# Kernel tuning notes

Measured on AMD Instinct MI355X. Metric: run time of the kernel, lower is better.

Reference implementation:

```python
import jax, jax.numpy as jnp
import numpy as np

SEED_THR = 0.5
DUP_THR = 0.8


def _connected_labels(adj):
    """Min-label propagation with pointer jumping; adj: [N,N] bool (diag set for active nodes)."""
    N = adj.shape[0]

    def cond(carry):
        _, changed = carry
        return changed

    def body(carry):
        labels, _ = carry
        nbr_min = jnp.min(jnp.where(adj, labels[None, :], N), axis=1)
        new = jnp.minimum(labels, nbr_min)
        new = jnp.minimum(new, new[new])  # pointer jumping -> O(log N) convergence
        return new, jnp.any(new != labels)

    labels0 = jnp.arange(N)
    labels, _ = jax.lax.while_loop(cond, body, (labels0, jnp.array(True)))
    return labels


def _per_image(sig, scores):
    # sig: [N,C], scores: [N]
    N = sig.shape[0]
    idx = jnp.arange(N)
    sel = scores >= SEED_THR
    # fallback: if nothing passes the threshold, select argmax score
    sel = jnp.where(sel.any(), sel, idx == jnp.argmax(scores))

    # cosine pairwise similarity
    sn = sig * jax.lax.rsqrt(jnp.sum(sig * sig, axis=-1, keepdims=True) + 1e-12)
    sim = sn @ sn.T  # [N,N]

    adj = (sim >= DUP_THR) & sel[:, None] & sel[None, :]
    adj = adj | jnp.diag(sel)  # diagonal True for selected nodes

    labels = _connected_labels(adj)  # component root = min node index in component

    neg_inf = jnp.float32(-1e30)
    masked_scores = jnp.where(sel, scores, neg_inf)
    comp_max = jnp.full((N,), neg_inf, dtype=scores.dtype).at[labels].max(masked_scores)
    is_best = sel & (scores >= comp_max[labels])
    # tie-break: smallest index (matches torch argmax-first semantics)
    comp_best = jnp.full((N,), N, dtype=jnp.int32).at[labels].min(
        jnp.where(is_best, idx, N).astype(jnp.int32))
    is_seed = sel & (idx == comp_best[labels])

    # compact seeds to the front, ordered by component root (== DFS discovery order)
    sort_key = jnp.where(is_seed, labels, N)
    order = jnp.argsort(sort_key)
    mask = is_seed[order]  # [N] bool, True for valid seed slots
    seed_sig = jnp.where(mask[:, None], sig[order], jnp.zeros((), sig.dtype))
    seed_sc = jnp.where(mask, scores[order], jnp.zeros((), scores.dtype))
    return seed_sig, mask, seed_sc


def reference(query_signatures, query_seed_logits):
    L, B, Q, C = query_signatures.shape
    sig = jnp.transpose(query_signatures, (1, 0, 2, 3)).reshape(B, L * Q, C)
    logits = jnp.transpose(query_seed_logits, (1, 0, 2)).reshape(B, L * Q).astype(jnp.float32)
    scores = jax.nn.sigmoid(logits)
    seed_signatures, pad_mask, seed_scores = jax.vmap(_per_image)(sig, scores)
    return seed_signatures, pad_mask, seed_scores


def setup_inputs() -> dict:
    key = jax.random.key(0)
    k1, k2 = jax.random.split(key)
    L, B, Q, C = 6, 4, 900, 256
    return {
        "query_signatures": jax.random.normal(k1, (L, B, Q, C), dtype=jnp.float32),
        "query_seed_logits": jax.random.normal(k2, (L, B, Q), dtype=jnp.float32),
    }
```

## Files before the change

kernel.cpp:

```cpp
#include <hip/hip_runtime.h>
#include <cstdint>
#include <cstddef>

#define LDIM 6
#define BDIM 4
#define QDIM 900
#define CDIM 256
#define NDIM (LDIM*QDIM)
#define NN   5408
#define T128 43
#define NT128 (T128*(T128+1)/2)

typedef float floatx4 __attribute__((ext_vector_type(4)));

__device__ __forceinline__ int sig_off(int b, int n) {
    int l = n / QDIM, q = n - l * QDIM;
    return ((l * BDIM + b) * QDIM + q) * CDIM;
}
__device__ __forceinline__ int logit_off(int b, int n) {
    int l = n / QDIM, q = n - l * QDIM;
    return (l * BDIM + b) * QDIM + q;
}

__device__ __forceinline__ int uf_load(const int* p, int i) {
    return __hip_atomic_load(&p[i], __ATOMIC_RELAXED, __HIP_MEMORY_SCOPE_AGENT);
}
__device__ int uf_find(int* p, int x) {
    int r = x;
    int pr = uf_load(p, r);
    while (pr != r) { r = pr; pr = uf_load(p, r); }
    return r;
}
__device__ void uf_union(int* p, int a, int b) {
    int ra = uf_find(p, a), rb = uf_find(p, b);
    while (ra != rb) {
        int hi = ra > rb ? ra : rb;
        int lo = ra ^ rb ^ hi;
        int old = atomicCAS(&p[hi], hi, lo);
        if (old == hi) return;
        ra = uf_find(p, old);
        rb = uf_find(p, lo);
    }
}

__device__ __forceinline__ int pk_fp8x4(float a, float b, float c, float d) {
    int p = __builtin_amdgcn_cvt_pk_fp8_f32(a, b, 0, false);
    p = __builtin_amdgcn_cvt_pk_fp8_f32(c, d, p, true);
    return p;
}

__global__ void k_init(const float* __restrict__ logits, float* __restrict__ scores,
                       int* __restrict__ parent, unsigned long long* __restrict__ compKey,
                       int* __restrict__ selIdx, int* __restrict__ Mcnt,
                       unsigned long long* __restrict__ argKey, int* __restrict__ done) {
    int b = blockIdx.y;
    int n = blockIdx.x * 256 + threadIdx.x;
    int lane = threadIdx.x & 63;
    if (n < NN) compKey[b * NN + n] = 0ULL;
    unsigned long long key = 0ULL;
    int f = 0;
    if (n < NDIM) {
        float x = logits[logit_off(b, n)];
        float sc = 1.0f / (1.0f + expf(-x));
        scores[b * NN + n] = sc;
        parent[b * NN + n] = n;
        f = (sc >= 0.5f) ? 1 : 0;
        key = ((unsigned long long)__float_as_uint(sc) << 32) | (unsigned int)(~n);
    }
    unsigned long long bal = __ballot(f != 0);
    int cnt = __popcll(bal);
    int rank = __popcll(bal & ((1ull << lane) - 1ull));
    int base = 0;
    if (lane == 0 && cnt) base = atomicAdd(&Mcnt[b], cnt);
    base = __shfl(base, 0);
    if (f) selIdx[b * NN + base + rank] = n;
    for (int off = 32; off; off >>= 1) {
        unsigned long long o = __shfl_down(key, off);
        if (o > key) key = o;
    }
    if (lane == 0) atomicMax(&argKey[b], key);
    __syncthreads();
    if (threadIdx.x == 0) {
        int prev = __hip_atomic_fetch_add(&done[b], 1, __ATOMIC_ACQ_REL,
                                          __HIP_MEMORY_SCOPE_AGENT);
        if (prev == (int)gridDim.x - 1) {
            if (__hip_atomic_load(&Mcnt[b], __ATOMIC_RELAXED, __HIP_MEMORY_SCOPE_AGENT) == 0) {
                unsigned long long k = __hip_atomic_load(&argKey[b], __ATOMIC_RELAXED,
                                                         __HIP_MEMORY_SCOPE_AGENT);
                selIdx[b * NN + 0] = (int)(~(unsigned int)(k & 0xffffffffULL));
                __hip_atomic_store(&Mcnt[b], 1, __ATOMIC_RELAXED, __HIP_MEMORY_SCOPE_AGENT);
            }
        }
    }
}

__global__ void k_tobf(const float* __restrict__ sig, const int* __restrict__ selIdx,
                       const int* __restrict__ Mcnt, char* __restrict__ Xf8) {
    int b = blockIdx.y;
    int g = (blockIdx.x * blockDim.x + threadIdx.x) >> 6;
    int lane = threadIdx.x & 63;
    if (g >= Mcnt[b]) return;
    int node = selIdx[b * NN + g];
    const float4 v = *(const float4*)(sig + sig_off(b, node) + lane * 4);
    float s = v.x * v.x + v.y * v.y + v.z * v.z + v.w * v.w;
    for (int off = 32; off; off >>= 1) s += __shfl_down(s, off);
    s = __shfl(s, 0);
    float ninv = rsqrtf(s + 1e-12f);
    int p = pk_fp8x4(v.x * ninv, v.y * ninv, v.z * ninv, v.w * ninv);
    int slot = (lane >> 2) ^ (g & 15);
    *(int*)(Xf8 + ((size_t)(b * NN + g)) * 256 + slot * 16 + (lane & 3) * 4) = p;
}

__global__ __launch_bounds__(256) void k_sim_mfma(const char* __restrict__ Xf8,
                                                  const int* __restrict__ selIdx,
                                                  const int* __restrict__ Mcnt,
                                                  int* __restrict__ parent) {
    int bx = blockIdx.x;
    int b = bx & 3;
    int t = bx >> 2;
    int M = Mcnt[b];
    int ti = (int)((sqrtf(8.0f * (float)t + 1.0f) - 1.0f) * 0.5f);
    while ((ti + 1) * (ti + 2) / 2 <= t) ti++;
    while (ti * (ti + 1) / 2 > t) ti--;
    int tj = t - ti * (ti + 1) / 2;
    if (ti * 128 >= M) return;

    extern __shared__ char Bs[];

    int tid = threadIdx.x;
    int lane = tid & 63, wave = tid >> 6;
    int rsel = lane & 15, quad = lane >> 4;

    const char* xb = Xf8 + ((size_t)b * NN) * 256;
#pragma unroll
    for (int k = 0; k < 8; k++) {
        int i = wave * 8 + k;
        int row = min(tj * 128 + 4 * i, NN - 4);
        const char* src = xb + (size_t)row * 256 + lane * 16;
        __builtin_amdgcn_global_load_lds(
            (const __attribute__((address_space(1))) unsigned int*)src,
            (__attribute__((address_space(3))) unsigned int*)(Bs + i * 1024),
            16, 0, 0);
    }

    int rA = ti * 128 + wave * 32;
    int gA0 = min(rA + rsel, M - 1);
    int gA1 = min(rA + 16 + rsel, M - 1);
    const char* pA0 = Xf8 + ((size_t)(b * NN + gA0)) * 256;
    const char* pA1 = Xf8 + ((size_t)(b * NN + gA1)) * 256;
    int swA0 = gA0 & 15, swA1 = gA1 & 15;

    __syncthreads();

    floatx4 acc[2][8];
#pragma unroll
    for (int s = 0; s < 2; s++)
#pragma unroll
        for (int nj = 0; nj < 8; nj++) acc[s][nj] = (floatx4){0.f, 0.f, 0.f, 0.f};

#pragma unroll
    for (int ks = 0; ks < 8; ks++) {
        int ch = ks * 2 + (quad >> 1);
        int ih = (quad & 1) * 8;
        long a0 = *(const long*)(pA0 + ((ch ^ swA0) << 4) + ih);
        long a1 = *(const long*)(pA1 + ((ch ^ swA1) << 4) + ih);
#pragma unroll
        for (int nj = 0; nj < 8; nj++) {
            int lr = nj * 16 + rsel;
            long bb = *(const long*)(Bs + lr * 256 + (((ch ^ (lr & 15)) << 4) + ih));
            acc[0][nj] = __builtin_amdgcn_mfma_f32_16x16x32_fp8_fp8(a0, bb, acc[0][nj], 0, 0, 0);
            acc[1][nj] = __builtin_amdgcn_mfma_f32_16x16x32_fp8_fp8(a1, bb, acc[1][nj], 0, 0, 0);
        }
    }

#pragma unroll
    for (int s = 0; s < 2; s++) {
        int rowA = rA + s * 16 + quad * 4;
#pragma unroll
        for (int nj = 0; nj < 8; nj++) {
            int gj = tj * 128 + nj * 16 + rsel;
#pragma unroll
            for (int r = 0; r < 4; r++) {
                int gi = rowA + r;
                if (gi < M && gj < M && gi > gj && acc[s][nj][r] >= 0.8f) {
                    uf_union(parent + b * NN, selIdx[b * NN + gi], selIdx[b * NN + gj]);
                }
            }
        }
    }
}

__global__ __launch_bounds__(1024) void k_comp(int* __restrict__ parent,
                                               const int* __restrict__ selIdx,
                                               const int* __restrict__ Mcnt,
                                               const float* __restrict__ scores,
                                               unsigned long long* __restrict__ compKey,
                                               int* __restrict__ seedNode,
                                               int* __restrict__ Scnt) {
    int b = blockIdx.x, t = threadIdx.x;
    int lane = t & 63, w = t >> 6;
    __shared__ int wsum[16];
    __shared__ int sbase;
    if (t == 0) sbase = 0;
    __syncthreads();

    int M = Mcnt[b];
    for (int base = 0; base < M; base += 1024) {
        int g = base + t;
        if (g < M) {
            int node = selIdx[b * NN + g];
            int root = uf_find(parent + b * NN, node);
            unsigned long long key =
                ((unsigned long long)__float_as_uint(scores[b * NN + node]) << 32) |
                (unsigned int)(~node);
            atomicMax(&compKey[b * NN + root], key);
        }
    }
    __syncthreads();

    for (int base = 0; base < NDIM; base += 1024) {
        int n = base + t;
        unsigned long long key = 0ULL;
        if (n < NDIM)
            key = __hip_atomic_load(&compKey[b * NN + n], __ATOMIC_RELAXED,
                                    __HIP_MEMORY_SCOPE_AGENT);
        int f = (key != 0ULL) ? 1 : 0;
        unsigned long long bal = __ballot(f != 0);
        int rank = __popcll(bal & ((1ull << lane) - 1ull));
        if (lane == 0) wsum[w] = __popcll(bal);
        __syncthreads();
        if (t == 0) {
            int s = sbase;
            for (int i = 0; i < 16; i++) { int v = wsum[i]; wsum[i] = s; s += v; }
            sbase = s;
        }
        __syncthreads();
        if (f) seedNode[b * NN + wsum[w] + rank] = (int)(~(unsigned int)(key & 0xffffffffULL));
        __syncthreads();
    }
    if (t == 0) Scnt[b] = sbase;
}

__global__ void k_write(const float* __restrict__ sig, const float* __restrict__ scores,
                        const int* __restrict__ seedNode, const int* __restrict__ Scnt,
                        float* __restrict__ out) {
    int b = blockIdx.y;
    int slot = blockIdx.x * 4 + (threadIdx.x >> 6);
    int lane = threadIdx.x & 63;
    float* orow = out + ((size_t)(b * NDIM + slot)) * CDIM + lane * 4;
    if (slot < Scnt[b]) {
        int s = seedNode[b * NN + slot];
        float4 v = *(const float4*)(sig + sig_off(b, s) + lane * 4);
        *(float4*)orow = v;
        if (lane == 0) {
            out[(size_t)BDIM * NDIM * CDIM + (size_t)b * NDIM + slot] = 1.0f;
            out[(size_t)BDIM * NDIM * CDIM + (size_t)BDIM * NDIM + (size_t)b * NDIM + slot] =
                scores[b * NN + s];
        }
    } else {
        float4 z = {0.f, 0.f, 0.f, 0.f};
        *(float4*)orow = z;
        if (lane == 0) {
            out[(size_t)BDIM * NDIM * CDIM + (size_t)b * NDIM + slot] = 0.0f;
            out[(size_t)BDIM * NDIM * CDIM + (size_t)BDIM * NDIM + (size_t)b * NDIM + slot] = 0.0f;
        }
    }
}

extern "C" void kernel_launch(void* const* d_in, const int* in_sizes, int n_in,
                              void* d_out, int out_size, void* d_ws, size_t ws_size,
                              hipStream_t stream) {
    (void)in_sizes; (void)n_in; (void)out_size; (void)ws_size;
    const float* sig = (const float*)d_in[0];
    const float* logits = (const float*)d_in[1];
    float* out = (float*)d_out;
    char* ws = (char*)d_ws;

    const size_t arr = (size_t)BDIM * NN * 4;
    int* Mcnt = (int*)(ws + 0);
    int* Scnt = (int*)(ws + 64);
    unsigned long long* argKey = (unsigned long long*)(ws + 128);
    int* done = (int*)(ws + 192);
    unsigned long long* compKey = (unsigned long long*)(ws + 256);
    float* scores = (float*)(ws + 256 + 2 * arr);
    int* parent   = (int*)(ws + 256 + 3 * arr);
    int* selIdx   = (int*)(ws + 256 + 4 * arr);
    int* seedNode = (int*)(ws + 256 + 5 * arr);
    char* Xf8     = (char*)(ws + 256 + 6 * arr);

    hipMemsetAsync(ws, 0, 512, stream);

    k_init<<<dim3((NN + 255) / 256, BDIM), 256, 0, stream>>>(
        logits, scores, parent, compKey, selIdx, Mcnt, argKey, done);
    k_tobf<<<dim3((NDIM + 3) / 4, BDIM), 256, 0, stream>>>(sig, selIdx, Mcnt, Xf8);
    k_sim_mfma<<<NT128 * BDIM, 256, 32768, stream>>>(Xf8, selIdx, Mcnt, parent);
    k_comp<<<BDIM, 1024, 0, stream>>>(parent, selIdx, Mcnt, scores, compKey, seedNode, Scnt);
    k_write<<<dim3(NDIM / 4, BDIM), 256, 0, stream>>>(sig, scores, seedNode, Scnt, out);
}
```

Before: 109.7 us.

## Fuse pipeline into one cooperative persistent kernel with grid syncs and bitmap compaction

Replaces the five-kernel launch sequence with a single cooperative kernel that runs init, fp8 normalization, MFMA similarity with union-find, component stats and the output write as phases separated by grid.sync. Seed compaction no longer uses a single-block serial scan per image. A bitmap of component roots is built instead, and each output row computes its slot with a popcount prefix. This is meant to remove launch gaps and the serialized k_comp stage, at the cost of grid-wide barriers, a persistent grid capped at 1024 blocks and redundant per-wave bitmap scans. The old multi-kernel path is kept as a fallback, with k_comp split into parallel k_stats plus a bitmap-based k_write.

```diff
diff --git a/kernel.cpp b/kernel.cpp
--- a/kernel.cpp
+++ b/kernel.cpp
@@ -1,6 +1,9 @@
 #include <hip/hip_runtime.h>
+#include <hip/hip_cooperative_groups.h>
 #include <cstdint>
 #include <cstddef>
+
+namespace cg = cooperative_groups;
 
 #define LDIM 6
 #define BDIM 4
@@ -49,14 +52,232 @@
     return p;
 }
 
+__device__ __forceinline__ void slot_write(const float* __restrict__ sig, float* __restrict__ out,
+                                           const unsigned long long* __restrict__ bm,
+                                           unsigned long long key, int b, int n, int lane) {
+    int W = n >> 6;
+    unsigned long long below = (1ull << (n & 63)) - 1ull;
+    unsigned long long w1 = __hip_atomic_load(&bm[lane], __ATOMIC_RELAXED,
+                                              __HIP_MEMORY_SCOPE_AGENT);
+    unsigned long long w2 = (lane < 21)
+        ? __hip_atomic_load(&bm[64 + lane], __ATOMIC_RELAXED, __HIP_MEMORY_SCOPE_AGENT) : 0ULL;
+    int t1 = __popcll(w1), t2 = __popcll(w2);
+    int p1 = (lane < W) ? t1 : ((lane == W) ? __popcll(w1 & below) : 0);
+    int l2 = 64 + lane;
+    int p2 = (l2 < W) ? t2 : ((l2 == W) ? __popcll(w2 & below) : 0);
+    unsigned long long packed =
+        ((unsigned long long)(t1 + t2) << 32) | (unsigned int)(p1 + p2);
+    for (int off = 32; off; off >>= 1) packed += __shfl_down(packed, off);
+    packed = __shfl(packed, 0);
+    int prefix = (int)(packed & 0xffffffffULL);
+    int S = (int)(packed >> 32);
+
+    int slot, node = 0;
+    float mk, scv;
+    if (key != 0ULL) {
+        slot = prefix;
+        node = (int)(~(unsigned int)key);
+        mk = 1.0f;
+        scv = __uint_as_float((unsigned int)(key >> 32));
+    } else {
+        slot = S + (n - prefix);
+        mk = 0.0f; scv = 0.0f;
+    }
+    float* orow = out + ((size_t)(b * NDIM + slot)) * CDIM + lane * 4;
+    if (key != 0ULL) {
+        *(float4*)orow = *(const float4*)(sig + sig_off(b, node) + lane * 4);
+    } else {
+        float4 z = {0.f, 0.f, 0.f, 0.f};
+        *(float4*)orow = z;
+    }
+    if (lane == 0) {
+        const size_t M0 = (size_t)BDIM * NDIM * CDIM;
+        out[M0 + (size_t)b * NDIM + slot] = mk;
+        out[M0 + (size_t)BDIM * NDIM + (size_t)b * NDIM + slot] = scv;
+    }
+}
+
+__global__ __launch_bounds__(256) void k_fused(
+    const float* __restrict__ sig, const float* __restrict__ logits,
+    float* __restrict__ out, float* __restrict__ scores, int* __restrict__ parent,
+    unsigned long long* __restrict__ compKey, int* __restrict__ selIdx,
+    int* __restrict__ Mcnt, unsigned long long* __restrict__ argKey,
+    int* __restrict__ done, unsigned long long* __restrict__ bitmap,
+    char* __restrict__ Xf8)
+{
+    cg::grid_group grid = cg::this_grid();
+    extern __shared__ char Bs[];
+
+    const int tid = threadIdx.x;
+    const int lane = tid & 63, wave = tid >> 6;
+    const int gidx = blockIdx.x * 256 + tid;
+    const int stride = gridDim.x * 256;
+    const int nwaves = gridDim.x * 4;
+    const int wgid = blockIdx.x * 4 + wave;
+
+    for (int i = gidx; i < BDIM * NN; i += stride) compKey[i] = 0ULL;
+    for (int i = gidx; i < BDIM * 128; i += stride) bitmap[i] = 0ULL;
+    for (int b = 0; b < BDIM; b++) {
+        int n = gidx;
+        int f = 0;
+        unsigned long long key = 0ULL;
+        if (n < NDIM) {
+            float x = logits[logit_off(b, n)];
+            float sc = 1.0f / (1.0f + expf(-x));
+            scores[b * NN + n] = sc;
+            parent[b * NN + n] = n;
+            f = (sc >= 0.5f) ? 1 : 0;
+            key = ((unsigned long long)__float_as_uint(sc) << 32) | (unsigned int)(~n);
+        }
+        unsigned long long bal = __ballot(f != 0);
+        int cnt = __popcll(bal);
+        int rank = __popcll(bal & ((1ull << lane) - 1ull));
+        int base = 0;
+        if (lane == 0 && cnt) base = atomicAdd(&Mcnt[b], cnt);
+        base = __shfl(base, 0);
+        if (f) selIdx[b * NN + base + rank] = n;
+        for (int off = 32; off; off >>= 1) {
+            unsigned long long o = __shfl_down(key, off);
+            if (o > key) key = o;
+        }
+        if (lane == 0 && key) atomicMax(&argKey[b], key);
+    }
+    __syncthreads();
+    if (tid == 0) {
+        int prev = __hip_atomic_fetch_add(done, 1, __ATOMIC_ACQ_REL,
+                                          __HIP_MEMORY_SCOPE_AGENT);
+        if (prev == (int)gridDim.x - 1) {
+            for (int b = 0; b < BDIM; b++) {
+                if (__hip_atomic_load(&Mcnt[b], __ATOMIC_RELAXED,
+                                      __HIP_MEMORY_SCOPE_AGENT) == 0) {
+                    unsigned long long k = __hip_atomic_load(&argKey[b], __ATOMIC_RELAXED,
+                                                             __HIP_MEMORY_SCOPE_AGENT);
+                    selIdx[b * NN + 0] = (int)(~(unsigned int)(k & 0xffffffffULL));
+                    __hip_atomic_store(&Mcnt[b], 1, __ATOMIC_RELAXED,
+                                       __HIP_MEMORY_SCOPE_AGENT);
+                }
+            }
+        }
+    }
+    grid.sync();
+
+    int M4[BDIM];
+    for (int b = 0; b < BDIM; b++)
+        M4[b] = __hip_atomic_load(&Mcnt[b], __ATOMIC_RELAXED, __HIP_MEMORY_SCOPE_AGENT);
+    for (int b = 0; b < BDIM; b++) {
+        for (int g = wgid; g < M4[b]; g += nwaves) {
+            int node = selIdx[b * NN + g];
+            const float4 v = *(const float4*)(sig + sig_off(b, node) + lane * 4);
+            float s = v.x * v.x + v.y * v.y + v.z * v.z + v.w * v.w;
+            for (int off = 32; off; off >>= 1) s += __shfl_down(s, off);
+            s = __shfl(s, 0);
+            float ninv = rsqrtf(s + 1e-12f);
+            int p = pk_fp8x4(v.x * ninv, v.y * ninv, v.z * ninv, v.w * ninv);
+            int slot = (lane >> 2) ^ (g & 15);
+            *(int*)(Xf8 + ((size_t)(b * NN + g)) * 256 + slot * 16 + (lane & 3) * 4) = p;
+        }
+    }
+    grid.sync();
+
+    const int rsel = lane & 15, quad = lane >> 4;
+    for (int tl = blockIdx.x; tl < NT128 * BDIM; tl += gridDim.x) {
+        int b = tl & 3, t = tl >> 2;
+        int M = M4[b];
+        int ti = (int)((sqrtf(8.0f * (float)t + 1.0f) - 1.0f) * 0.5f);
+        while ((ti + 1) * (ti + 2) / 2 <= t) ti++;
+        while (ti * (ti + 1) / 2 > t) ti--;
+        int tj = t - ti * (ti + 1) / 2;
+        if (ti * 128 >= M) continue;
+
+        __syncthreads();
+        const char* xb = Xf8 + ((size_t)b * NN) * 256;
+#pragma unroll
+        for (int k = 0; k < 8; k++) {
+            int i = wave * 8 + k;
+            int row = min(tj * 128 + 4 * i, NN - 4);
+            const char* src = xb + (size_t)row * 256 + lane * 16;
+            __builtin_amdgcn_global_load_lds(
+                (const __attribute__((address_space(1))) unsigned int*)src,
+                (__attribute__((address_space(3))) unsigned int*)(Bs + i * 1024),
+                16, 0, 0);
+        }
+        int rA = ti * 128 + wave * 32;
+        int gA0 = min(rA + rsel, M - 1);
+        int gA1 = min(rA + 16 + rsel, M - 1);
+        const char* pA0 = Xf8 + ((size_t)(b * NN + gA0)) * 256;
+        const char* pA1 = Xf8 + ((size_t)(b * NN + gA1)) * 256;
+        int swA0 = gA0 & 15, swA1 = gA1 & 15;
+        __syncthreads();
+
+        floatx4 acc[2][8];
+#pragma unroll
+        for (int s = 0; s < 2; s++)
+#pragma unroll
+            for (int nj = 0; nj < 8; nj++) acc[s][nj] = (floatx4){0.f, 0.f, 0.f, 0.f};
+#pragma unroll
+        for (int ks = 0; ks < 8; ks++) {
+            int ch = ks * 2 + (quad >> 1);
+            int ih = (quad & 1) * 8;
+            long a0 = *(const long*)(pA0 + ((ch ^ swA0) << 4) + ih);
+            long a1 = *(const long*)(pA1 + ((ch ^ swA1) << 4) + ih);
+#pragma unroll
+            for (int nj = 0; nj < 8; nj++) {
+                int lr = nj * 16 + rsel;
+                long bb = *(const long*)(Bs + lr * 256 + (((ch ^ (lr & 15)) << 4) + ih));
+                acc[0][nj] = __builtin_amdgcn_mfma_f32_16x16x32_fp8_fp8(a0, bb, acc[0][nj], 0, 0, 0);
+                acc[1][nj] = __builtin_amdgcn_mfma_f32_16x16x32_fp8_fp8(a1, bb, acc[1][nj], 0, 0, 0);
+            }
+        }
+#pragma unroll
+        for (int s = 0; s < 2; s++) {
+            int rowA = rA + s * 16 + quad * 4;
+#pragma unroll
+            for (int nj = 0; nj < 8; nj++) {
+                int gj = tj * 128 + nj * 16 + rsel;
+#pragma unroll
+                for (int r = 0; r < 4; r++) {
+                    int gi = rowA + r;
+                    if (gi < M && gj < M && gi > gj && acc[s][nj][r] >= 0.8f) {
+                        uf_union(parent + b * NN, selIdx[b * NN + gi], selIdx[b * NN + gj]);
+                    }
+                }
+            }
+        }
+    }
+    grid.sync();
+
+    for (int b = 0; b < BDIM; b++) {
+        for (int g = gidx; g < M4[b]; g += stride) {
+            int node = selIdx[b * NN + g];
+            int root = uf_find(parent + b * NN, node);
+            unsigned long long key =
+                ((unsigned long long)__float_as_uint(scores[b * NN + node]) << 32) |
+                (unsigned int)(~node);
+            atomicMax(&compKey[b * NN + root], key);
+            atomicOr(&bitmap[b * 128 + (root >> 6)], 1ull << (root & 63));
+        }
+    }
+    grid.sync();
+
+    for (int b = 0; b < BDIM; b++) {
+        for (int n = wgid; n < NDIM; n += nwaves) {
+            unsigned long long key = __hip_atomic_load(&compKey[b * NN + n], __ATOMIC_RELAXED,
+                                                       __HIP_MEMORY_SCOPE_AGENT);
+            slot_write(sig, out, bitmap + b * 128, key, b, n, lane);
+        }
+    }
+}
+
 __global__ void k_init(const float* __restrict__ logits, float* __restrict__ scores,
                        int* __restrict__ parent, unsigned long long* __restrict__ compKey,
-                       int* __restrict__ selIdx, int* __restrict__ Mcnt,
-                       unsigned long long* __restrict__ argKey, int* __restrict__ done) {
+                       unsigned long long* __restrict__ bitmap, int* __restrict__ selIdx,
+                       int* __restrict__ Mcnt, unsigned long long* __restrict__ argKey,
+                       int* __restrict__ done) {
     int b = blockIdx.y;
     int n = blockIdx.x * 256 + threadIdx.x;
     int lane = threadIdx.x & 63;
     if (n < NN) compKey[b * NN + n] = 0ULL;
+    if (n < 128) bitmap[b * 128 + n] = 0ULL;
     unsigned long long key = 0ULL;
     int f = 0;
     if (n < NDIM) {
@@ -78,7 +299,7 @@
         unsigned long long o = __shfl_down(key, off);
         if (o > key) key = o;
     }
-    if (lane == 0) atomicMax(&argKey[b], key);
+    if (lane == 0 && key) atomicMax(&argKey[b], key);
     __syncthreads();
     if (threadIdx.x == 0) {
         int prev = __hip_atomic_fetch_add(&done[b], 1, __ATOMIC_ACQ_REL,
@@ -126,7 +347,6 @@
     if (ti * 128 >= M) return;
 
     extern __shared__ char Bs[];
-
     int tid = threadIdx.x;
     int lane = tid & 63, wave = tid >> 6;
     int rsel = lane & 15, quad = lane >> 4;
@@ -142,14 +362,12 @@
             (__attribute__((address_space(3))) unsigned int*)(Bs + i * 1024),
             16, 0, 0);
     }
-
     int rA = ti * 128 + wave * 32;
     int gA0 = min(rA + rsel, M - 1);
     int gA1 = min(rA + 16 + rsel, M - 1);
     const char* pA0 = Xf8 + ((size_t)(b * NN + gA0)) * 256;
     const char* pA1 = Xf8 + ((size_t)(b * NN + gA1)) * 256;
     int swA0 = gA0 & 15, swA1 = gA1 & 15;
-
     __syncthreads();
 
     floatx4 acc[2][8];
@@ -157,7 +375,6 @@
     for (int s = 0; s < 2; s++)
 #pragma unroll
         for (int nj = 0; nj < 8; nj++) acc[s][nj] = (floatx4){0.f, 0.f, 0.f, 0.f};
-
 #pragma unroll
     for (int ks = 0; ks < 8; ks++) {
         int ch = ks * 2 + (quad >> 1);
@@ -172,7 +389,6 @@
             acc[1][nj] = __builtin_amdgcn_mfma_f32_16x16x32_fp8_fp8(a1, bb, acc[1][nj], 0, 0, 0);
         }
     }
-
 #pragma unroll
     for (int s = 0; s < 2; s++) {
         int rowA = rA + s * 16 + quad * 4;
@@ -190,81 +406,32 @@
     }
 }
 
-__global__ __launch_bounds__(1024) void k_comp(int* __restrict__ parent,
-                                               const int* __restrict__ selIdx,
-                                               const int* __restrict__ Mcnt,
-                                               const float* __restrict__ scores,
-                                               unsigned long long* __restrict__ compKey,
-                                               int* __restrict__ seedNode,
-                                               int* __restrict__ Scnt) {
-    int b = blockIdx.x, t = threadIdx.x;
-    int lane = t & 63, w = t >> 6;
-    __shared__ int wsum[16];
-    __shared__ int sbase;
-    if (t == 0) sbase = 0;
-    __syncthreads();
-
-    int M = Mcnt[b];
-    for (int base = 0; base < M; base += 1024) {
-        int g = base + t;
-        if (g < M) {
-            int node = selIdx[b * NN + g];
-            int root = uf_find(parent + b * NN, node);
-            unsigned long long key =
-                ((unsigned long long)__float_as_uint(scores[b * NN + node]) << 32) |
-                (unsigned int)(~node);
-            atomicMax(&compKey[b * NN + root], key);
-        }
-    }
-    __syncthreads();
-
-    for (int base = 0; base < NDIM; base += 1024) {
-        int n = base + t;
-        unsigned long long key = 0ULL;
-        if (n < NDIM)
-            key = __hip_atomic_load(&compKey[b * NN + n], __ATOMIC_RELAXED,
-                                    __HIP_MEMORY_SCOPE_AGENT);
-        int f = (key != 0ULL) ? 1 : 0;
-        unsigned long long bal = __ballot(f != 0);
-        int rank = __popcll(bal & ((1ull << lane) - 1ull));
-        if (lane == 0) wsum[w] = __popcll(bal);
-        __syncthreads();
-        if (t == 0) {
-            int s = sbase;
-            for (int i = 0; i < 16; i++) { int v = wsum[i]; wsum[i] = s; s += v; }
-            sbase = s;
-        }
-        __syncthreads();
-        if (f) seedNode[b * NN + wsum[w] + rank] = (int)(~(unsigned int)(key & 0xffffffffULL));
-        __syncthreads();
-    }
-    if (t == 0) Scnt[b] = sbase;
-}
-
-__global__ void k_write(const float* __restrict__ sig, const float* __restrict__ scores,
-                        const int* __restrict__ seedNode, const int* __restrict__ Scnt,
+__global__ void k_stats(int* __restrict__ parent, const int* __restrict__ selIdx,
+                        const int* __restrict__ Mcnt, const float* __restrict__ scores,
+                        unsigned long long* __restrict__ compKey,
+                        unsigned long long* __restrict__ bitmap) {
+    int b = blockIdx.y;
+    int g = blockIdx.x * 256 + threadIdx.x;
+    if (g >= Mcnt[b]) return;
+    int node = selIdx[b * NN + g];
+    int root = uf_find(parent + b * NN, node);
+    unsigned long long key =
+        ((unsigned long long)__float_as_uint(scores[b * NN + node]) << 32) |
+        (unsigned int)(~node);
+    atomicMax(&compKey[b * NN + root], key);
+    atomicOr(&bitmap[b * 128 + (root >> 6)], 1ull << (root & 63));
+}
+
+__global__ void k_write(const float* __restrict__ sig,
+                        const unsigned long long* __restrict__ compKey,
+                        const unsigned long long* __restrict__ bitmap,
                         float* __restrict__ out) {
     int b = blockIdx.y;
-    int slot = blockIdx.x * 4 + (threadIdx.x >> 6);
-    int lane = threadIdx.x & 63;
-    float* orow = out + ((size_t)(b * NDIM + slot)) * CDIM + lane * 4;
-    if (slot < Scnt[b]) {
-        int s = seedNode[b * NN + slot];
-        float4 v = *(const float4*)(sig + sig_off(b, s) + lane * 4);
-        *(float4*)orow = v;
-        if (lane == 0) {
-            out[(size_t)BDIM * NDIM * CDIM + (size_t)b * NDIM + slot] = 1.0f;
-            out[(size_t)BDIM * NDIM * CDIM + (size_t)BDIM * NDIM + (size_t)b * NDIM + slot] =
-                scores[b * NN + s];
-        }
-    } else {
-        float4 z = {0.f, 0.f, 0.f, 0.f};
-        *(float4*)orow = z;
-        if (lane == 0) {
-            out[(size_t)BDIM * NDIM * CDIM + (size_t)b * NDIM + slot] = 0.0f;
-            out[(size_t)BDIM * NDIM * CDIM + (size_t)BDIM * NDIM + (size_t)b * NDIM + slot] = 0.0f;
-        }
-    }
+    int wave = threadIdx.x >> 6, lane = threadIdx.x & 63;
+    int n = blockIdx.x * 4 + wave;
+    unsigned long long key = __hip_atomic_load(&compKey[b * NN + n], __ATOMIC_RELAXED,
+                                               __HIP_MEMORY_SCOPE_AGENT);
+    slot_write(sig, out, bitmap + b * 128, key, b, n, lane);
 }
 
 extern "C" void kernel_launch(void* const* d_in, const int* in_sizes, int n_in,
@@ -278,22 +445,36 @@
 
     const size_t arr = (size_t)BDIM * NN * 4;
     int* Mcnt = (int*)(ws + 0);
-    int* Scnt = (int*)(ws + 64);
-    unsigned long long* argKey = (unsigned long long*)(ws + 128);
-    int* done = (int*)(ws + 192);
-    unsigned long long* compKey = (unsigned long long*)(ws + 256);
-    float* scores = (float*)(ws + 256 + 2 * arr);
-    int* parent   = (int*)(ws + 256 + 3 * arr);
-    int* selIdx   = (int*)(ws + 256 + 4 * arr);
-    int* seedNode = (int*)(ws + 256 + 5 * arr);
-    char* Xf8     = (char*)(ws + 256 + 6 * arr);
-
-    hipMemsetAsync(ws, 0, 512, stream);
-
-    k_init<<<dim3((NN + 255) / 256, BDIM), 256, 0, stream>>>(
-        logits, scores, parent, compKey, selIdx, Mcnt, argKey, done);
-    k_tobf<<<dim3((NDIM + 3) / 4, BDIM), 256, 0, stream>>>(sig, selIdx, Mcnt, Xf8);
-    k_sim_mfma<<<NT128 * BDIM, 256, 32768, stream>>>(Xf8, selIdx, Mcnt, parent);
-    k_comp<<<BDIM, 1024, 0, stream>>>(parent, selIdx, Mcnt, scores, compKey, seedNode, Scnt);
-    k_write<<<dim3(NDIM / 4, BDIM), 256, 0, stream>>>(sig, scores, seedNode, Scnt, out);
-}
+    unsigned long long* argKey = (unsigned long long*)(ws + 64);
+    int* done = (int*)(ws + 128);
+    unsigned long long* bitmap = (unsigned long long*)(ws + 256);
+    unsigned long long* compKey = (unsigned long long*)(ws + 256 + 4096);
+    float* scores = (float*)(ws + 256 + 4096 + 2 * arr);
+    int* parent   = (int*)(ws + 256 + 4096 + 3 * arr);
+    int* selIdx   = (int*)(ws + 256 + 4096 + 4 * arr);
+    char* Xf8     = (char*)(ws + 256 + 4096 + 5 * arr);
+
+    hipMemsetAsync(ws, 0, 256, stream);
+
+    hipError_t err = hipErrorUnknown;
+    int nb = 0;
+    if (hipOccupancyMaxActiveBlocksPerMultiprocessor(&nb, k_fused, 256, 32768) == hipSuccess
+        && nb > 0) {
+        int grid = nb * 256;
+        if (grid > 1024) grid = 1024;
+        void* args[] = {(void*)&sig, (void*)&logits, (void*)&out, (void*)&scores,
+                        (void*)&parent, (void*)&compKey, (void*)&selIdx, (void*)&Mcnt,
+                        (void*)&argKey, (void*)&done, (void*)&bitmap, (void*)&Xf8};
+        err = hipLaunchCooperativeKernel((const void*)k_fused, dim3(grid), dim3(256),
+                                         args, 32768, stream);
+    }
+    if (err != hipSuccess) {
+        k_init<<<dim3((NN + 255) / 256, BDIM), 256, 0, stream>>>(
+            logits, scores, parent, compKey, bitmap, selIdx, Mcnt, argKey, done);
+        k_tobf<<<dim3((NDIM + 3) / 4, BDIM), 256, 0, stream>>>(sig, selIdx, Mcnt, Xf8);
+        k_sim_mfma<<<NT128 * BDIM, 256, 32768, stream>>>(Xf8, selIdx, Mcnt, parent);
+        k_stats<<<dim3((NDIM + 255) / 256, BDIM), 256, 0, stream>>>(
+            parent, selIdx, Mcnt, scores, compKey, bitmap);
+        k_write<<<dim3(NDIM / 4, BDIM), 256, 0, stream>>>(sig, compKey, bitmap, out);
+    }
+}
```

New measurement: 259.1 us. +136.2%, slower.

## Replace single-block component compaction with parallel stats kernel and bitmap-prefix writes

Applied to the files above, without the earlier changes.

Replaces the k_comp kernel, which ran one 1024-thread block per image and did a serial scan over all nodes, with a grid-wide k_stats kernel. k_stats does union-find lookups, atomicMax on the component keys, and sets bits in a per-image root bitmap. The write kernel now computes each output slot itself with a popcount prefix over the bitmap, for both seed and non-seed nodes, so the seedNode array and the separate scan are gone. This removes a low-parallelism serial step. In exchange, every wave reads the 85-word bitmap again and runs more atomics.

```diff
diff --git a/kernel.cpp b/kernel.cpp
--- a/kernel.cpp
+++ b/kernel.cpp
@@ -49,14 +49,61 @@
     return p;
 }
 
+__device__ __forceinline__ void slot_write(const float* __restrict__ sig, float* __restrict__ out,
+                                           const unsigned long long* __restrict__ bm,
+                                           unsigned long long key, int b, int n, int lane) {
+    int W = n >> 6;
+    unsigned long long below = (1ull << (n & 63)) - 1ull;
+    unsigned long long w1 = __hip_atomic_load(&bm[lane], __ATOMIC_RELAXED,
+                                              __HIP_MEMORY_SCOPE_AGENT);
+    unsigned long long w2 = (lane < 21)
+        ? __hip_atomic_load(&bm[64 + lane], __ATOMIC_RELAXED, __HIP_MEMORY_SCOPE_AGENT) : 0ULL;
+    int t1 = __popcll(w1), t2 = __popcll(w2);
+    int p1 = (lane < W) ? t1 : ((lane == W) ? __popcll(w1 & below) : 0);
+    int l2 = 64 + lane;
+    int p2 = (l2 < W) ? t2 : ((l2 == W) ? __popcll(w2 & below) : 0);
+    unsigned long long packed =
+        ((unsigned long long)(t1 + t2) << 32) | (unsigned int)(p1 + p2);
+    for (int off = 32; off; off >>= 1) packed += __shfl_down(packed, off);
+    packed = __shfl(packed, 0);
+    int prefix = (int)(packed & 0xffffffffULL);
+    int S = (int)(packed >> 32);
+
+    int slot, node = 0;
+    float mk, scv;
+    if (key != 0ULL) {
+        slot = prefix;
+        node = (int)(~(unsigned int)key);
+        mk = 1.0f;
+        scv = __uint_as_float((unsigned int)(key >> 32));
+    } else {
+        slot = S + (n - prefix);
+        mk = 0.0f; scv = 0.0f;
+    }
+    float* orow = out + ((size_t)(b * NDIM + slot)) * CDIM + lane * 4;
+    if (key != 0ULL) {
+        *(float4*)orow = *(const float4*)(sig + sig_off(b, node) + lane * 4);
+    } else {
+        float4 z = {0.f, 0.f, 0.f, 0.f};
+        *(float4*)orow = z;
+    }
+    if (lane == 0) {
+        const size_t M0 = (size_t)BDIM * NDIM * CDIM;
+        out[M0 + (size_t)b * NDIM + slot] = mk;
+        out[M0 + (size_t)BDIM * NDIM + (size_t)b * NDIM + slot] = scv;
+    }
+}
+
 __global__ void k_init(const float* __restrict__ logits, float* __restrict__ scores,
                        int* __restrict__ parent, unsigned long long* __restrict__ compKey,
-                       int* __restrict__ selIdx, int* __restrict__ Mcnt,
-                       unsigned long long* __restrict__ argKey, int* __restrict__ done) {
+                       unsigned long long* __restrict__ bitmap, int* __restrict__ selIdx,
+                       int* __restrict__ Mcnt, unsigned long long* __restrict__ argKey,
+                       int* __restrict__ done) {
     int b = blockIdx.y;
     int n = blockIdx.x * 256 + threadIdx.x;
     int lane = threadIdx.x & 63;
     if (n < NN) compKey[b * NN + n] = 0ULL;
+    if (n < 128) bitmap[b * 128 + n] = 0ULL;
     unsigned long long key = 0ULL;
     int f = 0;
     if (n < NDIM) {
@@ -78,7 +125,7 @@
         unsigned long long o = __shfl_down(key, off);
         if (o > key) key = o;
     }
-    if (lane == 0) atomicMax(&argKey[b], key);
+    if (lane == 0 && key) atomicMax(&argKey[b], key);
     __syncthreads();
     if (threadIdx.x == 0) {
         int prev = __hip_atomic_fetch_add(&done[b], 1, __ATOMIC_ACQ_REL,
@@ -126,7 +173,6 @@
     if (ti * 128 >= M) return;
 
     extern __shared__ char Bs[];
-
     int tid = threadIdx.x;
     int lane = tid & 63, wave = tid >> 6;
     int rsel = lane & 15, quad = lane >> 4;
@@ -142,14 +188,12 @@
             (__attribute__((address_space(3))) unsigned int*)(Bs + i * 1024),
             16, 0, 0);
     }
-
     int rA = ti * 128 + wave * 32;
     int gA0 = min(rA + rsel, M - 1);
     int gA1 = min(rA + 16 + rsel, M - 1);
     const char* pA0 = Xf8 + ((size_t)(b * NN + gA0)) * 256;
     const char* pA1 = Xf8 + ((size_t)(b * NN + gA1)) * 256;
     int swA0 = gA0 & 15, swA1 = gA1 & 15;
-
     __syncthreads();
 
     floatx4 acc[2][8];
@@ -157,7 +201,6 @@
     for (int s = 0; s < 2; s++)
 #pragma unroll
         for (int nj = 0; nj < 8; nj++) acc[s][nj] = (floatx4){0.f, 0.f, 0.f, 0.f};
-
 #pragma unroll
     for (int ks = 0; ks < 8; ks++) {
         int ch = ks * 2 + (quad >> 1);
@@ -172,7 +215,6 @@
             acc[1][nj] = __builtin_amdgcn_mfma_f32_16x16x32_fp8_fp8(a1, bb, acc[1][nj], 0, 0, 0);
         }
     }
-
 #pragma unroll
     for (int s = 0; s < 2; s++) {
         int rowA = rA + s * 16 + quad * 4;
@@ -190,81 +232,32 @@
     }
 }
 
-__global__ __launch_bounds__(1024) void k_comp(int* __restrict__ parent,
-                                               const int* __restrict__ selIdx,
-                                               const int* __restrict__ Mcnt,
-                                               const float* __restrict__ scores,
-                                               unsigned long long* __restrict__ compKey,
-                                               int* __restrict__ seedNode,
-                                               int* __restrict__ Scnt) {
-    int b = blockIdx.x, t = threadIdx.x;
-    int lane = t & 63, w = t >> 6;
-    __shared__ int wsum[16];
-    __shared__ int sbase;
-    if (t == 0) sbase = 0;
-    __syncthreads();
-
-    int M = Mcnt[b];
-    for (int base = 0; base < M; base += 1024) {
-        int g = base + t;
-        if (g < M) {
-            int node = selIdx[b * NN + g];
-            int root = uf_find(parent + b * NN, node);
-            unsigned long long key =
-                ((unsigned long long)__float_as_uint(scores[b * NN + node]) << 32) |
-                (unsigned int)(~node);
-            atomicMax(&compKey[b * NN + root], key);
-        }
-    }
-    __syncthreads();
-
-    for (int base = 0; base < NDIM; base += 1024) {
-        int n = base + t;
-        unsigned long long key = 0ULL;
-        if (n < NDIM)
-            key = __hip_atomic_load(&compKey[b * NN + n], __ATOMIC_RELAXED,
-                                    __HIP_MEMORY_SCOPE_AGENT);
-        int f = (key != 0ULL) ? 1 : 0;
-        unsigned long long bal = __ballot(f != 0);
-        int rank = __popcll(bal & ((1ull << lane) - 1ull));
-        if (lane == 0) wsum[w] = __popcll(bal);
-        __syncthreads();
-        if (t == 0) {
-            int s = sbase;
-            for (int i = 0; i < 16; i++) { int v = wsum[i]; wsum[i] = s; s += v; }
-            sbase = s;
-        }
-        __syncthreads();
-        if (f) seedNode[b * NN + wsum[w] + rank] = (int)(~(unsigned int)(key & 0xffffffffULL));
-        __syncthreads();
-    }
-    if (t == 0) Scnt[b] = sbase;
-}
-
-__global__ void k_write(const float* __restrict__ sig, const float* __restrict__ scores,
-                        const int* __restrict__ seedNode, const int* __restrict__ Scnt,
+__global__ void k_stats(int* __restrict__ parent, const int* __restrict__ selIdx,
+                        const int* __restrict__ Mcnt, const float* __restrict__ scores,
+                        unsigned long long* __restrict__ compKey,
+                        unsigned long long* __restrict__ bitmap) {
+    int b = blockIdx.y;
+    int g = blockIdx.x * 256 + threadIdx.x;
+    if (g >= Mcnt[b]) return;
+    int node = selIdx[b * NN + g];
+    int root = uf_find(parent + b * NN, node);
+    unsigned long long key =
+        ((unsigned long long)__float_as_uint(scores[b * NN + node]) << 32) |
+        (unsigned int)(~node);
+    atomicMax(&compKey[b * NN + root], key);
+    atomicOr(&bitmap[b * 128 + (root >> 6)], 1ull << (root & 63));
+}
+
+__global__ void k_write(const float* __restrict__ sig,
+                        const unsigned long long* __restrict__ compKey,
+                        const unsigned long long* __restrict__ bitmap,
                         float* __restrict__ out) {
     int b = blockIdx.y;
-    int slot = blockIdx.x * 4 + (threadIdx.x >> 6);
-    int lane = threadIdx.x & 63;
-    float* orow = out + ((size_t)(b * NDIM + slot)) * CDIM + lane * 4;
-    if (slot < Scnt[b]) {
-        int s = seedNode[b * NN + slot];
-        float4 v = *(const float4*)(sig + sig_off(b, s) + lane * 4);
-        *(float4*)orow = v;
-        if (lane == 0) {
-            out[(size_t)BDIM * NDIM * CDIM + (size_t)b * NDIM + slot] = 1.0f;
-            out[(size_t)BDIM * NDIM * CDIM + (size_t)BDIM * NDIM + (size_t)b * NDIM + slot] =
-                scores[b * NN + s];
-        }
-    } else {
-        float4 z = {0.f, 0.f, 0.f, 0.f};
-        *(float4*)orow = z;
-        if (lane == 0) {
-            out[(size_t)BDIM * NDIM * CDIM + (size_t)b * NDIM + slot] = 0.0f;
-            out[(size_t)BDIM * NDIM * CDIM + (size_t)BDIM * NDIM + (size_t)b * NDIM + slot] = 0.0f;
-        }
-    }
+    int wave = threadIdx.x >> 6, lane = threadIdx.x & 63;
+    int n = blockIdx.x * 4 + wave;
+    unsigned long long key = __hip_atomic_load(&compKey[b * NN + n], __ATOMIC_RELAXED,
+                                               __HIP_MEMORY_SCOPE_AGENT);
+    slot_write(sig, out, bitmap + b * 128, key, b, n, lane);
 }
 
 extern "C" void kernel_launch(void* const* d_in, const int* in_sizes, int n_in,
@@ -278,22 +271,22 @@
 
     const size_t arr = (size_t)BDIM * NN * 4;
     int* Mcnt = (int*)(ws + 0);
-    int* Scnt = (int*)(ws + 64);
-    unsigned long long* argKey = (unsigned long long*)(ws + 128);
-    int* done = (int*)(ws + 192);
-    unsigned long long* compKey = (unsigned long long*)(ws + 256);
-    float* scores = (float*)(ws + 256 + 2 * arr);
-    int* parent   = (int*)(ws + 256 + 3 * arr);
-    int* selIdx   = (int*)(ws + 256 + 4 * arr);
-    int* seedNode = (int*)(ws + 256 + 5 * arr);
-    char* Xf8     = (char*)(ws + 256 + 6 * arr);
-
-    hipMemsetAsync(ws, 0, 512, stream);
+    unsigned long long* argKey = (unsigned long long*)(ws + 64);
+    int* done = (int*)(ws + 128);
+    unsigned long long* bitmap = (unsigned long long*)(ws + 256);
+    unsigned long long* compKey = (unsigned long long*)(ws + 256 + 4096);
+    float* scores = (float*)(ws + 256 + 4096 + 2 * arr);
+    int* parent   = (int*)(ws + 256 + 4096 + 3 * arr);
+    int* selIdx   = (int*)(ws + 256 + 4096 + 4 * arr);
+    char* Xf8     = (char*)(ws + 256 + 4096 + 5 * arr);
+
+    hipMemsetAsync(ws, 0, 256, stream);
 
     k_init<<<dim3((NN + 255) / 256, BDIM), 256, 0, stream>>>(
-        logits, scores, parent, compKey, selIdx, Mcnt, argKey, done);
+        logits, scores, parent, compKey, bitmap, selIdx, Mcnt, argKey, done);
     k_tobf<<<dim3((NDIM + 3) / 4, BDIM), 256, 0, stream>>>(sig, selIdx, Mcnt, Xf8);
     k_sim_mfma<<<NT128 * BDIM, 256, 32768, stream>>>(Xf8, selIdx, Mcnt, parent);
-    k_comp<<<BDIM, 1024, 0, stream>>>(parent, selIdx, Mcnt, scores, compKey, seedNode, Scnt);
-    k_write<<<dim3(NDIM / 4, BDIM), 256, 0, stream>>>(sig, scores, seedNode, Scnt, out);
-}
+    k_stats<<<dim3((NDIM + 255) / 256, BDIM), 256, 0, stream>>>(
+        parent, selIdx, Mcnt, scores, compKey, bitmap);
+    k_write<<<dim3(NDIM / 4, BDIM), 256, 0, stream>>>(sig, compKey, bitmap, out);
+}
```

After: 111.6 us. Within noise of the previous version (+1.7%).
